# Optimization experiments

Hardware: AMD Instinct MI355X
Metric: run time of the kernel (lower is better)

## Reference

```python
import jax, jax.numpy as jnp
import numpy as np

# ---- problem sizes ----
CNO = 10000        # constant_no
PAD = 10001        # padding_idx (also used as the 'variable' marker in queries)
KS = max(CNO, PAD) + 2   # key_scale / pack_base = 10003
N_PRED = 128
F = 2_000_000
B = 200_000


def _build_segment_index(keys: np.ndarray, max_key: int):
    """numpy replica of torch _build_segment_index: (order, starts, lens)."""
    order = np.argsort(keys, kind='stable')
    uniq, counts = np.unique(keys, return_counts=True)  # unique keys, sorted
    starts = np.zeros(max_key, dtype=np.int64)
    lens = np.zeros(max_key, dtype=np.int64)
    cum = np.cumsum(counts)
    starts[uniq] = cum - counts
    lens[uniq] = counts
    return order, starts, lens


def setup_inputs() -> dict:
    rng = np.random.default_rng(0)
    # facts: [F,3] (pred, arg0, arg1), constants in [1, CNO]
    fp = rng.integers(0, N_PRED, F)
    fa0 = rng.integers(1, CNO + 1, F)
    fa1 = rng.integers(1, CNO + 1, F)
    # FactIndex.__init__ sorts facts by packed hash before building indices
    hashes = (fp.astype(np.int64) * KS + fa0) * KS + fa1
    h_order = np.argsort(hashes, kind='stable')
    fp, fa0, fa1 = fp[h_order], fa0[h_order], fa1[h_order]
    # three segment indexes: (pred,arg0), (pred,arg1), pred-only
    k0 = fp.astype(np.int64) * KS + fa0
    k1 = fp.astype(np.int64) * KS + fa1
    o0, s0, l0 = _build_segment_index(k0, int(k0.max()) + 1)
    o1, s1, l1 = _build_segment_index(k1, int(k1.max()) + 1)
    op, sp, lp = _build_segment_index(fp.astype(np.int64), int(fp.max()) + 1)
    # queries: 1/3 (pred,const,var), 1/3 (pred,var,const), 1/3 (pred,var,var)
    qp = rng.integers(0, N_PRED, B)
    pattern = rng.integers(0, 3, B)
    c0 = rng.integers(1, CNO + 1, B)
    c1 = rng.integers(1, CNO + 1, B)
    qa0 = np.where(pattern == 0, c0, PAD)
    qa1 = np.where(pattern == 1, c1, PAD)
    query_atoms = np.stack([qp, qa0, qa1], axis=1)
    ja = lambda a: jnp.asarray(a, dtype=jnp.int32)
    return {
        'query_atoms': ja(query_atoms),
        'a0_order': ja(o0), 'a0_starts': ja(s0), 'a0_lens': ja(l0),
        'a1_order': ja(o1), 'a1_starts': ja(s1), 'a1_lens': ja(l1),
        'p_order': ja(op), 'p_starts': ja(sp), 'p_lens': ja(lp),
        'max_results': 64,
    }


def reference(query_atoms, a0_order, a0_starts, a0_lens,
              a1_order, a1_starts, a1_lens,
              p_order, p_starts, p_lens, max_results):
    B = query_atoms.shape[0]
    F = a0_order.shape[0]
    clamp_max = max(F - 1, 0)
    preds = query_atoms[:, 0]
    a0 = query_atoms[:, 1]
    a1 = query_atoms[:, 2]
    is_c0 = (a0 <= CNO) & (a0 != PAD)
    is_c1 = (a1 <= CNO) & (a1 != PAD)
    offsets = jnp.arange(max_results, dtype=jnp.int32)[None, :]  # [1,K]

    def _lookup(order, starts, lens, keys, is_const):
        safe = jnp.clip(keys, 0, starts.shape[0] - 1)
        left = starts[safe]                                  # [B]
        cnt = jnp.minimum(lens[safe], max_results)           # [B]
        idx = jnp.clip(left[:, None] + offsets, 0, clamp_max)  # [B,K]
        v = (offsets < cnt[:, None]) & is_const[:, None]
        return order[idx], v

    fi0, v0 = _lookup(a0_order, a0_starts, a0_lens, preds * KS + a0, is_c0)
    fi1, v1 = _lookup(a1_order, a1_starts, a1_lens, preds * KS + a1, is_c1)
    use0 = is_c0[:, None]
    fact_idx = jnp.where(use0, fi0, fi1)
    valid = jnp.where(use0, v0, v1)
    # pred-only fallback when both args are variables
    both_var = (~is_c0) & (~is_c1) & (preds != PAD)
    fip, vp = _lookup(p_order, p_starts, p_lens, preds, both_var)
    bv = both_var[:, None]
    fact_idx = jnp.where(bv, fip, fact_idx)
    valid = jnp.where(bv, vp, valid)
    return fact_idx, valid
```

## Files before the change

### kernel.cpp

```cpp
#include <hip/hip_runtime.h>

#define CNO_C 10000
#define PAD_C 10001
#define KS_C  10003

__global__ __launch_bounds__(256) void akfi_block64(
    const int* __restrict__ qa,
    const int* __restrict__ o0, const int* __restrict__ s0, const int* __restrict__ l0,
    const int* __restrict__ o1, const int* __restrict__ s1, const int* __restrict__ l1,
    const int* __restrict__ op, const int* __restrict__ sp, const int* __restrict__ lp,
    int n0, int n1, int npred,
    int F, int B,
    int* __restrict__ out_idx,
    int* __restrict__ out_valid)
{
    __shared__ int4 desc[256];

    const int tid   = threadIdx.x;
    const int qbase = blockIdx.x << 8;

    {
        int q = qbase + tid;
        if (q < B) {
            int p  = qa[q * 3 + 0];
            int a0 = qa[q * 3 + 1];
            int a1 = qa[q * 3 + 2];

            bool is_c0 = (a0 <= CNO_C) && (a0 != PAD_C);
            bool is_c1 = (a1 <= CNO_C) && (a1 != PAD_C);
            bool both  = (!is_c0) && (!is_c1) && (p != PAD_C);

            const int* starts; const int* lens;
            int key, nsz, tbl; bool isc;
            if (is_c0)      { starts = s0; lens = l0; key = p * KS_C + a0; nsz = n0;    isc = true;  tbl = 0; }
            else if (both)  { starts = sp; lens = lp; key = p;             nsz = npred; isc = true;  tbl = 1; }
            else            { starts = s1; lens = l1; key = p * KS_C + a1; nsz = n1;    isc = is_c1; tbl = 2; }

            int safe = min(max(key, 0), nsz - 1);
            int left = starts[safe];
            int cnt  = min(lens[safe], 64);
            int cnt_eff = isc ? cnt : 0;

            desc[tid] = make_int4(left, cnt_eff, tbl, 0);
        }
    }
    __syncthreads();

    const int lq  = tid >> 4;
    const int j4  = (tid & 15) << 2;
    const int Fm1 = F - 1;

#pragma unroll 4
    for (int i = 0; i < 16; ++i) {
        int qq = lq + (i << 4);
        int q  = qbase + qq;
        if (q >= B) continue;

        int4 d = desc[qq];
        const int* order = (d.z == 0) ? o0 : (d.z == 1) ? op : o1;

        int idx0 = d.x + j4;
        int f0, f1, f2, f3;
        if (idx0 >= 0 && idx0 + 3 <= Fm1) {
            f0 = order[idx0];
            f1 = order[idx0 + 1];
            f2 = order[idx0 + 2];
            f3 = order[idx0 + 3];
        } else {
            f0 = order[min(max(idx0,     0), Fm1)];
            f1 = order[min(max(idx0 + 1, 0), Fm1)];
            f2 = order[min(max(idx0 + 2, 0), Fm1)];
            f3 = order[min(max(idx0 + 3, 0), Fm1)];
        }

        int cnt = d.y;
        int4 fv = make_int4(f0, f1, f2, f3);
        int4 vv = make_int4(j4 < cnt ? 1 : 0,
                            j4 + 1 < cnt ? 1 : 0,
                            j4 + 2 < cnt ? 1 : 0,
                            j4 + 3 < cnt ? 1 : 0);

        long long ob = ((long long)q << 6) + j4;
        *reinterpret_cast<int4*>(out_idx + ob)   = fv;
        *reinterpret_cast<int4*>(out_valid + ob) = vv;
    }
}

__global__ __launch_bounds__(256) void akfi_vec4(
    const int* __restrict__ qa,
    const int* __restrict__ o0, const int* __restrict__ s0, const int* __restrict__ l0,
    const int* __restrict__ o1, const int* __restrict__ s1, const int* __restrict__ l1,
    const int* __restrict__ op, const int* __restrict__ sp, const int* __restrict__ lp,
    int n0, int n1, int npred,
    int F, int B, int mr,
    int* __restrict__ out_idx,
    int* __restrict__ out_valid)
{
    long long t = (long long)blockIdx.x * blockDim.x + threadIdx.x;
    int per_q = mr >> 2;
    long long total = (long long)B * per_q;
    if (t >= total) return;

    int q = (int)(t / per_q), j4 = (int)(t % per_q) << 2;

    int p  = qa[q * 3 + 0];
    int a0 = qa[q * 3 + 1];
    int a1 = qa[q * 3 + 2];
    bool is_c0 = (a0 <= CNO_C) && (a0 != PAD_C);
    bool is_c1 = (a1 <= CNO_C) && (a1 != PAD_C);
    bool both  = (!is_c0) && (!is_c1) && (p != PAD_C);

    const int* order; const int* starts; const int* lens;
    int key, nsz; bool isc;
    if (is_c0)      { order = o0; starts = s0; lens = l0; key = p * KS_C + a0; nsz = n0;    isc = true;  }
    else if (both)  { order = op; starts = sp; lens = lp; key = p;             nsz = npred; isc = true;  }
    else            { order = o1; starts = s1; lens = l1; key = p * KS_C + a1; nsz = n1;    isc = is_c1; }

    int safe = min(max(key, 0), nsz - 1);
    int left = starts[safe];
    int cnt  = min(lens[safe], mr);
    if (!isc) cnt = 0;
    int Fm1 = F - 1;

    int idx0 = left + j4;
    int f0, f1, f2, f3;
    if (idx0 >= 0 && idx0 + 3 <= Fm1) {
        f0 = order[idx0]; f1 = order[idx0 + 1]; f2 = order[idx0 + 2]; f3 = order[idx0 + 3];
    } else {
        f0 = order[min(max(idx0,     0), Fm1)];
        f1 = order[min(max(idx0 + 1, 0), Fm1)];
        f2 = order[min(max(idx0 + 2, 0), Fm1)];
        f3 = order[min(max(idx0 + 3, 0), Fm1)];
    }

    int4 fv = make_int4(f0, f1, f2, f3);
    int4 vv = make_int4(j4 < cnt ? 1 : 0, j4 + 1 < cnt ? 1 : 0,
                        j4 + 2 < cnt ? 1 : 0, j4 + 3 < cnt ? 1 : 0);
    long long ob = (long long)q * mr + j4;
    *reinterpret_cast<int4*>(out_idx + ob)   = fv;
    *reinterpret_cast<int4*>(out_valid + ob) = vv;
}

__global__ __launch_bounds__(256) void akfi_scalar(
    const int* __restrict__ qa,
    const int* __restrict__ o0, const int* __restrict__ s0, const int* __restrict__ l0,
    const int* __restrict__ o1, const int* __restrict__ s1, const int* __restrict__ l1,
    const int* __restrict__ op, const int* __restrict__ sp, const int* __restrict__ lp,
    int n0, int n1, int npred,
    int F, int B, int mr,
    int* __restrict__ out_idx,
    int* __restrict__ out_valid)
{
    long long t = (long long)blockIdx.x * blockDim.x + threadIdx.x;
    long long total = (long long)B * (long long)mr;
    if (t >= total) return;
    int q = (int)(t / mr), j = (int)(t % mr);

    int p  = qa[q * 3 + 0];
    int a0 = qa[q * 3 + 1];
    int a1 = qa[q * 3 + 2];
    bool is_c0 = (a0 <= CNO_C) && (a0 != PAD_C);
    bool is_c1 = (a1 <= CNO_C) && (a1 != PAD_C);
    bool both  = (!is_c0) && (!is_c1) && (p != PAD_C);

    const int* order; const int* starts; const int* lens;
    int key, nsz; bool isc;
    if (is_c0)      { order = o0; starts = s0; lens = l0; key = p * KS_C + a0; nsz = n0;    isc = true;  }
    else if (both)  { order = op; starts = sp; lens = lp; key = p;             nsz = npred; isc = true;  }
    else            { order = o1; starts = s1; lens = l1; key = p * KS_C + a1; nsz = n1;    isc = is_c1; }

    int safe = min(max(key, 0), nsz - 1);
    int left = starts[safe];
    int cnt  = min(lens[safe], mr);
    int idx  = min(max(left + j, 0), F - 1);

    long long ob = (long long)q * mr + j;
    out_idx[ob]   = order[idx];
    out_valid[ob] = (isc && j < cnt) ? 1 : 0;
}

extern "C" void kernel_launch(void* const* d_in, const int* in_sizes, int n_in,
                              void* d_out, int out_size, void* d_ws, size_t ws_size,
                              hipStream_t stream) {
    const int* qa = (const int*)d_in[0];
    const int* o0 = (const int*)d_in[1];
    const int* s0 = (const int*)d_in[2];
    const int* l0 = (const int*)d_in[3];
    const int* o1 = (const int*)d_in[4];
    const int* s1 = (const int*)d_in[5];
    const int* l1 = (const int*)d_in[6];
    const int* op = (const int*)d_in[7];
    const int* sp = (const int*)d_in[8];
    const int* lp = (const int*)d_in[9];
    int B  = in_sizes[0] / 3;
    int F  = in_sizes[1];
    int n0 = in_sizes[2];
    int n1 = in_sizes[5];
    int npred = in_sizes[8];
    int mr = out_size / (2 * B);

    int* out_idx   = (int*)d_out;
    int* out_valid = (int*)d_out + (long long)B * mr;

    int block = 256;
    if (mr == 64) {
        int blocks = (B + 255) / 256;
        akfi_block64<<<blocks, block, 0, stream>>>(
            qa, o0, s0, l0, o1, s1, l1, op, sp, lp,
            n0, n1, npred, F, B, out_idx, out_valid);
    } else if ((mr & 3) == 0) {
        long long total = (long long)B * (mr >> 2);
        int blocks = (int)((total + block - 1) / block);
        akfi_vec4<<<blocks, block, 0, stream>>>(
            qa, o0, s0, l0, o1, s1, l1, op, sp, lp,
            n0, n1, npred, F, B, mr, out_idx, out_valid);
    } else {
        long long total = (long long)B * (long long)mr;
        int blocks = (int)((total + block - 1) / block);
        akfi_scalar<<<blocks, block, 0, stream>>>(
            qa, o0, s0, l0, o1, s1, l1, op, sp, lp,
            n0, n1, npred, F, B, mr, out_idx, out_valid);
    }
}
```

Measured before the change: 35.00 us.

## Replace shared-descriptor block kernel with flat 8-wide per-thread kernel using nontemporal stores

The mr==64 path drops the shared-memory descriptor stage and its barrier. Instead each thread handles 8 consecutive outputs of one query and recomputes that query's segment lookup, with 8 threads per query. Output writes become nontemporal 16-byte vector stores, meant to avoid polluting cache with the 100MB write stream. This trades redundant per-query lookups (8x instead of 1x) for more parallelism, no synchronization and a larger per-thread gather.

```diff
diff --git a/kernel.cpp b/kernel.cpp
--- a/kernel.cpp
+++ b/kernel.cpp
@@ -4,7 +4,9 @@
 #define PAD_C 10001
 #define KS_C  10003
 
-__global__ __launch_bounds__(256) void akfi_block64(
+typedef int iv4 __attribute__((ext_vector_type(4)));
+
+__global__ __launch_bounds__(256) void akfi_vec8(
     const int* __restrict__ qa,
     const int* __restrict__ o0, const int* __restrict__ s0, const int* __restrict__ l0,
     const int* __restrict__ o1, const int* __restrict__ s1, const int* __restrict__ l1,
@@ -14,76 +16,55 @@
     int* __restrict__ out_idx,
     int* __restrict__ out_valid)
 {
-    __shared__ int4 desc[256];
-
-    const int tid   = threadIdx.x;
-    const int qbase = blockIdx.x << 8;
-
-    {
-        int q = qbase + tid;
-        if (q < B) {
-            int p  = qa[q * 3 + 0];
-            int a0 = qa[q * 3 + 1];
-            int a1 = qa[q * 3 + 2];
-
-            bool is_c0 = (a0 <= CNO_C) && (a0 != PAD_C);
-            bool is_c1 = (a1 <= CNO_C) && (a1 != PAD_C);
-            bool both  = (!is_c0) && (!is_c1) && (p != PAD_C);
-
-            const int* starts; const int* lens;
-            int key, nsz, tbl; bool isc;
-            if (is_c0)      { starts = s0; lens = l0; key = p * KS_C + a0; nsz = n0;    isc = true;  tbl = 0; }
-            else if (both)  { starts = sp; lens = lp; key = p;             nsz = npred; isc = true;  tbl = 1; }
-            else            { starts = s1; lens = l1; key = p * KS_C + a1; nsz = n1;    isc = is_c1; tbl = 2; }
-
-            int safe = min(max(key, 0), nsz - 1);
-            int left = starts[safe];
-            int cnt  = min(lens[safe], 64);
-            int cnt_eff = isc ? cnt : 0;
-
-            desc[tid] = make_int4(left, cnt_eff, tbl, 0);
-        }
+    long long t = (long long)blockIdx.x * blockDim.x + threadIdx.x;
+    long long total = (long long)B * 8;
+    if (t >= total) return;
+
+    int q  = (int)(t >> 3);
+    int j8 = (int)(t & 7) << 3;
+
+    int p  = qa[q * 3 + 0];
+    int a0 = qa[q * 3 + 1];
+    int a1 = qa[q * 3 + 2];
+
+    bool is_c0 = (a0 <= CNO_C) && (a0 != PAD_C);
+    bool is_c1 = (a1 <= CNO_C) && (a1 != PAD_C);
+    bool both  = (!is_c0) && (!is_c1) && (p != PAD_C);
+
+    const int* order; const int* starts; const int* lens;
+    int key, nsz; bool isc;
+    if (is_c0)      { order = o0; starts = s0; lens = l0; key = p * KS_C + a0; nsz = n0;    isc = true;  }
+    else if (both)  { order = op; starts = sp; lens = lp; key = p;             nsz = npred; isc = true;  }
+    else            { order = o1; starts = s1; lens = l1; key = p * KS_C + a1; nsz = n1;    isc = is_c1; }
+
+    int safe = min(max(key, 0), nsz - 1);
+    int left = starts[safe];
+    int cnt  = min(lens[safe], 64);
+    if (!isc) cnt = 0;
+    const int Fm1 = F - 1;
+
+    int idx0 = left + j8;
+    int f[8];
+    if (idx0 >= 0 && idx0 + 7 <= Fm1) {
+#pragma unroll
+        for (int e = 0; e < 8; ++e) f[e] = order[idx0 + e];
+    } else {
+#pragma unroll
+        for (int e = 0; e < 8; ++e) f[e] = order[min(max(idx0 + e, 0), Fm1)];
     }
-    __syncthreads();
-
-    const int lq  = tid >> 4;
-    const int j4  = (tid & 15) << 2;
-    const int Fm1 = F - 1;
-
-#pragma unroll 4
-    for (int i = 0; i < 16; ++i) {
-        int qq = lq + (i << 4);
-        int q  = qbase + qq;
-        if (q >= B) continue;
-
-        int4 d = desc[qq];
-        const int* order = (d.z == 0) ? o0 : (d.z == 1) ? op : o1;
-
-        int idx0 = d.x + j4;
-        int f0, f1, f2, f3;
-        if (idx0 >= 0 && idx0 + 3 <= Fm1) {
-            f0 = order[idx0];
-            f1 = order[idx0 + 1];
-            f2 = order[idx0 + 2];
-            f3 = order[idx0 + 3];
-        } else {
-            f0 = order[min(max(idx0,     0), Fm1)];
-            f1 = order[min(max(idx0 + 1, 0), Fm1)];
-            f2 = order[min(max(idx0 + 2, 0), Fm1)];
-            f3 = order[min(max(idx0 + 3, 0), Fm1)];
-        }
-
-        int cnt = d.y;
-        int4 fv = make_int4(f0, f1, f2, f3);
-        int4 vv = make_int4(j4 < cnt ? 1 : 0,
-                            j4 + 1 < cnt ? 1 : 0,
-                            j4 + 2 < cnt ? 1 : 0,
-                            j4 + 3 < cnt ? 1 : 0);
-
-        long long ob = ((long long)q << 6) + j4;
-        *reinterpret_cast<int4*>(out_idx + ob)   = fv;
-        *reinterpret_cast<int4*>(out_valid + ob) = vv;
-    }
+
+    iv4 fv0 = (iv4){f[0], f[1], f[2], f[3]};
+    iv4 fv1 = (iv4){f[4], f[5], f[6], f[7]};
+    iv4 vv0 = (iv4){j8     < cnt ? 1 : 0, j8 + 1 < cnt ? 1 : 0,
+                    j8 + 2 < cnt ? 1 : 0, j8 + 3 < cnt ? 1 : 0};
+    iv4 vv1 = (iv4){j8 + 4 < cnt ? 1 : 0, j8 + 5 < cnt ? 1 : 0,
+                    j8 + 6 < cnt ? 1 : 0, j8 + 7 < cnt ? 1 : 0};
+
+    long long ob = ((long long)q << 6) + j8;
+    __builtin_nontemporal_store(fv0, reinterpret_cast<iv4*>(out_idx + ob));
+    __builtin_nontemporal_store(fv1, reinterpret_cast<iv4*>(out_idx + ob + 4));
+    __builtin_nontemporal_store(vv0, reinterpret_cast<iv4*>(out_valid + ob));
+    __builtin_nontemporal_store(vv1, reinterpret_cast<iv4*>(out_valid + ob + 4));
 }
 
 __global__ __launch_bounds__(256) void akfi_vec4(
@@ -133,12 +114,12 @@
         f3 = order[min(max(idx0 + 3, 0), Fm1)];
     }
 
-    int4 fv = make_int4(f0, f1, f2, f3);
-    int4 vv = make_int4(j4 < cnt ? 1 : 0, j4 + 1 < cnt ? 1 : 0,
-                        j4 + 2 < cnt ? 1 : 0, j4 + 3 < cnt ? 1 : 0);
+    iv4 fv = (iv4){f0, f1, f2, f3};
+    iv4 vv = (iv4){j4 < cnt ? 1 : 0, j4 + 1 < cnt ? 1 : 0,
+                   j4 + 2 < cnt ? 1 : 0, j4 + 3 < cnt ? 1 : 0};
     long long ob = (long long)q * mr + j4;
-    *reinterpret_cast<int4*>(out_idx + ob)   = fv;
-    *reinterpret_cast<int4*>(out_valid + ob) = vv;
+    *reinterpret_cast<iv4*>(out_idx + ob)   = fv;
+    *reinterpret_cast<iv4*>(out_valid + ob) = vv;
 }
 
 __global__ __launch_bounds__(256) void akfi_scalar(
@@ -204,8 +185,9 @@
 
     int block = 256;
     if (mr == 64) {
-        int blocks = (B + 255) / 256;
-        akfi_block64<<<blocks, block, 0, stream>>>(
+        long long total = (long long)B * 8;
+        int blocks = (int)((total + block - 1) / block);
+        akfi_vec8<<<blocks, block, 0, stream>>>(
             qa, o0, s0, l0, o1, s1, l1, op, sp, lp,
             n0, n1, npred, F, B, out_idx, out_valid);
     } else if ((mr & 3) == 0) {
```

Result: slower. 62.38 us (+78.2%).
